# Kernel optimization log

Measured on AMD Instinct MI355X. Metric: run time of the kernel, lower is better.

## Reference

```python
import jax, jax.numpy as jnp
import numpy as np

N, E, D, T = 10000, 320000, 128, 128


def _layer_norm(x, g, b, eps=1e-5):
    mu = jnp.mean(x, axis=-1, keepdims=True)
    var = jnp.mean(jnp.square(x - mu), axis=-1, keepdims=True)
    return (x - mu) * jax.lax.rsqrt(var + eps) * g + b


def setup_inputs() -> dict:
    key = jax.random.key(0)
    ks = jax.random.split(key, 24)
    s = 0.05

    def lin(k, fin, fout):
        k1, k2 = jax.random.split(k)
        return (jax.random.normal(k1, (fin, fout), jnp.float32) * s,
                jax.random.normal(k2, (fout,), jnp.float32) * s)

    W_tp, b_tp = lin(ks[5], T, D)
    W_sg, b_sg = lin(ks[6], D, D)
    W_dg, b_dg = lin(ks[7], D, D)
    W_eg, b_eg = lin(ks[8], D, D)
    W_su, b_su = lin(ks[9], D, D)
    W_du, b_du = lin(ks[10], D, D)
    return {
        'node_feats': jax.random.normal(ks[0], (N, D), jnp.float32),
        'edge_feats': jax.random.normal(ks[1], (E, D), jnp.float32),
        'time_feats': jax.random.normal(ks[2], (N, T), jnp.float32),
        'src': jax.random.randint(ks[3], (E,), 0, N),
        'dst': jax.random.randint(ks[4], (E,), 0, N),
        'W_tp': W_tp, 'b_tp': b_tp,
        'W_sg': W_sg, 'b_sg': b_sg,
        'W_dg': W_dg, 'b_dg': b_dg,
        'W_eg': W_eg, 'b_eg': b_eg,
        'W_su': W_su, 'b_su': b_su,
        'W_du': W_du, 'b_du': b_du,
        'ln_e_g': jnp.ones((D,), jnp.float32), 'ln_e_b': jnp.zeros((D,), jnp.float32),
        'ln_n_g': jnp.ones((D,), jnp.float32), 'ln_n_b': jnp.zeros((D,), jnp.float32),
    }


def reference(node_feats, edge_feats, time_feats, src, dst,
              W_tp, b_tp, W_sg, b_sg, W_dg, b_dg, W_eg, b_eg,
              W_su, b_su, W_du, b_du, ln_e_g, ln_e_b, ln_n_g, ln_n_b):
    n_nodes = node_feats.shape[0]
    # per-node gate projections (time proj folded into source gate)
    e_src = node_feats @ W_sg + b_sg + time_feats @ W_tp + b_tp   # [N, D]
    e_dst = node_feats @ W_dg + b_dg                              # [N, D]
    # edge gating: gather from both endpoints + edge feature projection
    m = e_src[src] + e_dst[dst] + edge_feats @ W_eg + b_eg        # [E, D]
    sigma = jax.nn.sigmoid(m)                                     # [E, D]
    # gated message passing: scatter-add over destination nodes
    Bh = node_feats @ W_du + b_du                                 # [N, D]
    sum_sigma_h = jax.ops.segment_sum(Bh[src] * sigma, dst, num_segments=n_nodes)
    sum_sigma = jax.ops.segment_sum(sigma, dst, num_segments=n_nodes)
    h = sum_sigma_h / (sum_sigma + 1e-6)                          # [N, D]
    x = node_feats @ W_su + b_su + h
    x = jax.nn.silu(_layer_norm(x, ln_n_g, ln_n_b))
    y = jax.nn.silu(_layer_norm(m, ln_e_g, ln_e_b))
    x = node_feats + x  # residual
    y = edge_feats + y
    return (x, y)
```

## Files before the change

### kernel.cpp

```cpp
#include <hip/hip_runtime.h>
#include <hip/hip_bf16.h>

#define N_NODES 10000
#define N_EDGES 320000
#define D 128
#define NBINS 10000

typedef float f32x4 __attribute__((ext_vector_type(4)));
typedef float f32x2 __attribute__((ext_vector_type(2)));
typedef short bf16x8 __attribute__((ext_vector_type(8)));

static __device__ inline short f2bf(float f) {
    union { __hip_bfloat16 h; short s; } u;
    u.h = __float2bfloat16(f);
    return u.s;
}

static __device__ inline float bf2f(short s) {
    union { float f; unsigned u; } x;
    x.u = ((unsigned)(unsigned short)s) << 16;
    return x.f;
}

static __device__ inline float fast_rcp(float x) { return __builtin_amdgcn_rcpf(x); }

__global__ void prepack_kernel(const float* __restrict__ W0, const float* __restrict__ W1,
                               short* __restrict__ out, int K) {
    int idx = blockIdx.x * 256 + threadIdx.x;
    if (idx >= K * 128) return;
    int b  = idx & 7;
    int l  = (idx >> 3) & 63;
    int jt = (idx >> 9) & 7;
    int t  = idx >> 12;
    int k = 32 * t + ((l >> 4) * 8) + b;
    int j = jt * 16 + (l & 15);
    float v = (k < 128) ? W0[k * 128 + j] : W1[(k - 128) * 128 + j];
    out[idx] = f2bf(v);
}

__global__ void hist_kernel(const int* __restrict__ dst, int* __restrict__ cnt) {
    int i = blockIdx.x * 256 + threadIdx.x;
    if (i < N_EDGES) atomicAdd(&cnt[dst[i]], 1);
}

__launch_bounds__(1024)
__global__ void scan_kernel(const int* __restrict__ cnt, int* __restrict__ cursor) {
    __shared__ int s[1024];
    int t = threadIdx.x;
    int b0 = t * 10;
    int loc[10];
    int tot = 0;
#pragma unroll
    for (int i = 0; i < 10; ++i) {
        int v = (b0 + i < NBINS) ? cnt[b0 + i] : 0;
        loc[i] = tot; tot += v;
    }
    s[t] = tot;
    __syncthreads();
    for (int off = 1; off < 1024; off <<= 1) {
        int v = (t >= off) ? s[t - off] : 0;
        __syncthreads();
        s[t] += v;
        __syncthreads();
    }
    int base = (t == 0) ? 0 : s[t - 1];
#pragma unroll
    for (int i = 0; i < 10; ++i)
        if (b0 + i < NBINS) cursor[b0 + i] = base + loc[i];
}

__global__ void scatter_kernel(const int* __restrict__ dst, int* __restrict__ cursor,
                               int* __restrict__ perm) {
    int i = blockIdx.x * 256 + threadIdx.x;
    if (i < N_EDGES) {
        int p = atomicAdd(&cursor[dst[i]], 1);
        perm[p] = i;
    }
}

__launch_bounds__(256)
__global__ void node_proj_kernel(const float* __restrict__ node,
                                 const float* __restrict__ timef,
                                 const short* __restrict__ Wsrc_pk,
                                 const short* __restrict__ Wdg_pk,
                                 const short* __restrict__ Wdu_pk,
                                 const short* __restrict__ Wsu_pk,
                                 const float* __restrict__ b_sg, const float* __restrict__ b_tp,
                                 const float* __restrict__ b_dg, const float* __restrict__ b_du,
                                 const float* __restrict__ b_su, const float* __restrict__ b_eg,
                                 short* __restrict__ spk,
                                 short* __restrict__ dpk,
                                 float* __restrict__ xs) {
    int tid = threadIdx.x;
    int w = tid >> 6;
    int l = tid & 63;
    int g = l >> 4;
    int lr = l & 15;
    int r0 = blockIdx.x * 64 + w * 16;
    int arow = r0 + lr;

    bf16x8 aN[4], aT[4];
    if (arow < N_NODES) {
        const float* np = node + (size_t)arow * D;
        const float* tp = timef + (size_t)arow * D;
#pragma unroll
        for (int t = 0; t < 4; ++t) {
            int k0 = 32 * t + g * 8;
            f32x4 v0 = *(const f32x4*)(np + k0);
            f32x4 v1 = *(const f32x4*)(np + k0 + 4);
            f32x4 u0 = *(const f32x4*)(tp + k0);
            f32x4 u1 = *(const f32x4*)(tp + k0 + 4);
            bf16x8 a, b;
#pragma unroll
            for (int i = 0; i < 4; ++i) {
                a[i] = f2bf(v0[i]); a[4 + i] = f2bf(v1[i]);
                b[i] = f2bf(u0[i]); b[4 + i] = f2bf(u1[i]);
            }
            aN[t] = a; aT[t] = b;
        }
    } else {
        bf16x8 z = {0, 0, 0, 0, 0, 0, 0, 0};
#pragma unroll
        for (int t = 0; t < 4; ++t) { aN[t] = z; aT[t] = z; }
    }

    const bf16x8* Bsrc = (const bf16x8*)Wsrc_pk;
    const bf16x8* Bdg  = (const bf16x8*)Wdg_pk;
    const bf16x8* Bdu  = (const bf16x8*)Wdu_pk;
    const bf16x8* Bsu  = (const bf16x8*)Wsu_pk;

#pragma unroll
    for (int jt = 0; jt < 8; ++jt) {
        int c = jt * 16 + lr;
        f32x4 acc = {0.f, 0.f, 0.f, 0.f};
#pragma unroll
        for (int t = 0; t < 4; ++t)
            acc = __builtin_amdgcn_mfma_f32_16x16x32_bf16(aN[t], Bsrc[(t * 8 + jt) * 64 + l], acc, 0, 0, 0);
#pragma unroll
        for (int t = 0; t < 4; ++t)
            acc = __builtin_amdgcn_mfma_f32_16x16x32_bf16(aT[t], Bsrc[((4 + t) * 8 + jt) * 64 + l], acc, 0, 0, 0);
        float bias = b_sg[c] + b_tp[c];
#pragma unroll
        for (int r = 0; r < 4; ++r) {
            int row = r0 + g * 4 + r;
            if (row < N_NODES) spk[(size_t)row * 256 + c] = f2bf(acc[r] + bias);
        }
    }

#pragma unroll
    for (int jt = 0; jt < 8; ++jt) {
        int c = jt * 16 + lr;
        f32x4 a0 = {0.f, 0.f, 0.f, 0.f}, a1 = a0, a2 = a0;
#pragma unroll
        for (int t = 0; t < 4; ++t) {
            a0 = __builtin_amdgcn_mfma_f32_16x16x32_bf16(aN[t], Bdg[(t * 8 + jt) * 64 + l], a0, 0, 0, 0);
            a1 = __builtin_amdgcn_mfma_f32_16x16x32_bf16(aN[t], Bdu[(t * 8 + jt) * 64 + l], a1, 0, 0, 0);
            a2 = __builtin_amdgcn_mfma_f32_16x16x32_bf16(aN[t], Bsu[(t * 8 + jt) * 64 + l], a2, 0, 0, 0);
        }
        float bdgc = b_dg[c] + b_eg[c];
        float bdu = b_du[c], bsu = b_su[c];
#pragma unroll
        for (int r = 0; r < 4; ++r) {
            int row = r0 + g * 4 + r;
            if (row < N_NODES) {
                dpk[(size_t)row * D + c]       = f2bf(a0[r] + bdgc);
                spk[(size_t)row * 256 + 128 + c] = f2bf(a1[r] + bdu);
                xs[(size_t)row * D + c]        = a2[r] + bsu;
            }
        }
    }
}

__launch_bounds__(256)
__global__ void edge_kernel(const float* __restrict__ edgef,
                            const int* __restrict__ src, const int* __restrict__ dst,
                            const int* __restrict__ perm,
                            const short* __restrict__ Weg_pk,
                            const short* __restrict__ spk,
                            const short* __restrict__ dpk,
                            const float* __restrict__ ln_g, const float* __restrict__ ln_b,
                            float* __restrict__ ss, float* __restrict__ ssh,
                            float* __restrict__ y) {
    __shared__ short Bs[128 * 128];
    {
        const bf16x8* gw = (const bf16x8*)Weg_pk;
        bf16x8* sw = (bf16x8*)Bs;
        for (int i = threadIdx.x; i < 2048; i += 256) sw[i] = gw[i];
    }
    __syncthreads();

    int tid = threadIdx.x;
    int w = tid >> 6;
    int l = tid & 63;
    int g = l >> 4;
    int lr = l & 15;
    int b = blockIdx.x;
    int swz = (b & 7) * 625 + (b >> 3);
    int e0 = swz * 64 + w * 16;

    int eA = perm[e0 + lr];
    int eidx[4], sidx[4], didx[4];
#pragma unroll
    for (int r = 0; r < 4; ++r) {
        eidx[r] = perm[e0 + g * 4 + r];
        sidx[r] = src[eidx[r]];
        didx[r] = dst[eidx[r]];
    }

    bf16x8 aE[4];
    {
        const float* ep = edgef + (size_t)eA * D;
#pragma unroll
        for (int t = 0; t < 4; ++t) {
            int k0 = 32 * t + g * 8;
            f32x4 v0 = *(const f32x4*)(ep + k0);
            f32x4 v1 = *(const f32x4*)(ep + k0 + 4);
            bf16x8 a;
#pragma unroll
            for (int i = 0; i < 4; ++i) { a[i] = f2bf(v0[i]); a[4 + i] = f2bf(v1[i]); }
            aE[t] = a;
        }
    }

    const bf16x8* Bp = (const bf16x8*)Bs;
    f32x4 acc[8];
#pragma unroll
    for (int jt = 0; jt < 8; ++jt) {
        f32x4 c4 = {0.f, 0.f, 0.f, 0.f};
#pragma unroll
        for (int t = 0; t < 4; ++t)
            c4 = __builtin_amdgcn_mfma_f32_16x16x32_bf16(aE[t], Bp[(t * 8 + jt) * 64 + l], c4, 0, 0, 0);
        acc[jt] = c4;
    }

    int dfirst = __shfl(didx[0], 0);
    int dlast  = __shfl(didx[3], 48);
    bool uniform = (dfirst == dlast);

    float gcol[8], bbcol[8];
#pragma unroll
    for (int jt = 0; jt < 8; ++jt) {
        int c = jt * 16 + lr;
        gcol[jt] = ln_g[c]; bbcol[jt] = ln_b[c];
    }

    float sum[4] = {0.f, 0.f, 0.f, 0.f}, sq[4] = {0.f, 0.f, 0.f, 0.f};
#pragma unroll
    for (int jt = 0; jt < 8; ++jt) {
        int c = jt * 16 + lr;
        float sg[4], bsg[4];
#pragma unroll
        for (int r = 0; r < 4; ++r) {
            float es = bf2f(spk[(size_t)sidx[r] * 256 + c]);
            float bh = bf2f(spk[(size_t)sidx[r] * 256 + 128 + c]);
            float ed = bf2f(dpk[(size_t)didx[r] * D + c]);
            float m = acc[jt][r] + es + ed;
            acc[jt][r] = m;
            float s = fast_rcp(1.f + __expf(-m));
            sg[r] = s;
            bsg[r] = bh * s;
            sum[r] += m; sq[r] += m * m;
        }
        if (uniform) {
            float aS = (sg[0] + sg[1]) + (sg[2] + sg[3]);
            float aH = (bsg[0] + bsg[1]) + (bsg[2] + bsg[3]);
            aS += __shfl_xor(aS, 16); aH += __shfl_xor(aH, 16);
            aS += __shfl_xor(aS, 32); aH += __shfl_xor(aH, 32);
            if (g == 0) {
                atomicAdd(&ss [(size_t)dfirst * D + c], aS);
                atomicAdd(&ssh[(size_t)dfirst * D + c], aH);
            }
        } else {
            float aS = sg[0], aH = bsg[0];
#pragma unroll
            for (int r = 1; r < 4; ++r) {
                if (didx[r] == didx[r - 1]) { aS += sg[r]; aH += bsg[r]; }
                else {
                    atomicAdd(&ss [(size_t)didx[r - 1] * D + c], aS);
                    atomicAdd(&ssh[(size_t)didx[r - 1] * D + c], aH);
                    aS = sg[r]; aH = bsg[r];
                }
            }
            atomicAdd(&ss [(size_t)didx[3] * D + c], aS);
            atomicAdd(&ssh[(size_t)didx[3] * D + c], aH);
        }
    }

#pragma unroll
    for (int r = 0; r < 4; ++r) {
        float s = sum[r], q = sq[r];
#pragma unroll
        for (int mk = 1; mk < 16; mk <<= 1) { s += __shfl_xor(s, mk); q += __shfl_xor(q, mk); }
        float mean = s * (1.f / D);
        float var = q * (1.f / D) - mean * mean;
        sum[r] = mean;
        sq[r] = rsqrtf(var + 1e-5f);
    }

#pragma unroll
    for (int jt = 0; jt < 8; ++jt) {
        int c = jt * 16 + lr;
#pragma unroll
        for (int r = 0; r < 4; ++r) {
            float v = (acc[jt][r] - sum[r]) * sq[r] * gcol[jt] + bbcol[jt];
            float sl = v * fast_rcp(1.f + __expf(-v));
            size_t off = (size_t)eidx[r] * D + c;
            y[off] = edgef[off] + sl;
        }
    }
}

__launch_bounds__(256)
__global__ void node_out_kernel(const float* __restrict__ node,
                                const float* __restrict__ xs,
                                const float* __restrict__ ssh, const float* __restrict__ ss,
                                const float* __restrict__ ln_g, const float* __restrict__ ln_b,
                                float* __restrict__ x) {
    int w = threadIdx.x >> 6;
    int l = threadIdx.x & 63;
    int row = blockIdx.x * 4 + w;
    if (row >= N_NODES) return;
    size_t base = (size_t)row * D + 2 * l;
    f32x2 xv = *(const f32x2*)(xs + base);
    f32x2 hs = *(const f32x2*)(ssh + base);
    f32x2 sv = *(const f32x2*)(ss + base);
    float v0 = xv[0] + hs[0] / (sv[0] + 1e-6f);
    float v1 = xv[1] + hs[1] / (sv[1] + 1e-6f);
    float s = v0 + v1, q = v0 * v0 + v1 * v1;
#pragma unroll
    for (int mk = 1; mk < 64; mk <<= 1) { s += __shfl_xor(s, mk); q += __shfl_xor(q, mk); }
    float mean = s * (1.f / D);
    float var = q * (1.f / D) - mean * mean;
    float rstd = rsqrtf(var + 1e-5f);
    float t0 = (v0 - mean) * rstd * ln_g[2 * l] + ln_b[2 * l];
    float t1 = (v1 - mean) * rstd * ln_g[2 * l + 1] + ln_b[2 * l + 1];
    t0 = t0 * fast_rcp(1.f + __expf(-t0));
    t1 = t1 * fast_rcp(1.f + __expf(-t1));
    f32x2 nv = *(const f32x2*)(node + base);
    f32x2 outv;
    outv[0] = nv[0] + t0;
    outv[1] = nv[1] + t1;
    *(f32x2*)(x + base) = outv;
}

extern "C" void kernel_launch(void* const* d_in, const int* in_sizes, int n_in,
                              void* d_out, int out_size, void* d_ws, size_t ws_size,
                              hipStream_t stream) {
    const float* node  = (const float*)d_in[0];
    const float* edgef = (const float*)d_in[1];
    const float* timef = (const float*)d_in[2];
    const int*   src   = (const int*)d_in[3];
    const int*   dst   = (const int*)d_in[4];
    const float* W_tp = (const float*)d_in[5];  const float* b_tp = (const float*)d_in[6];
    const float* W_sg = (const float*)d_in[7];  const float* b_sg = (const float*)d_in[8];
    const float* W_dg = (const float*)d_in[9];  const float* b_dg = (const float*)d_in[10];
    const float* W_eg = (const float*)d_in[11]; const float* b_eg = (const float*)d_in[12];
    const float* W_su = (const float*)d_in[13]; const float* b_su = (const float*)d_in[14];
    const float* W_du = (const float*)d_in[15]; const float* b_du = (const float*)d_in[16];
    const float* ln_e_g = (const float*)d_in[17]; const float* ln_e_b = (const float*)d_in[18];
    const float* ln_n_g = (const float*)d_in[19]; const float* ln_n_b = (const float*)d_in[20];

    char* ws = (char*)d_ws;
    size_t nd = (size_t)N_NODES * D;
    float* ss    = (float*)ws; ws += nd * 4;
    float* ssh   = (float*)ws; ws += nd * 4;
    float* xs    = (float*)ws; ws += nd * 4;
    short* spk   = (short*)ws; ws += (size_t)N_NODES * 256 * 2;
    short* dpk   = (short*)ws; ws += nd * 2;
    short* Wsrc_pk = (short*)ws; ws += 256 * 128 * 2;
    short* Wdg_pk  = (short*)ws; ws += 128 * 128 * 2;
    short* Wdu_pk  = (short*)ws; ws += 128 * 128 * 2;
    short* Wsu_pk  = (short*)ws; ws += 128 * 128 * 2;
    short* Weg_pk  = (short*)ws; ws += 128 * 128 * 2;
    int* cnt       = (int*)ws; ws += 10240 * 4;
    int* cursor    = (int*)ws; ws += 10240 * 4;
    int* perm      = (int*)ws; ws += (size_t)N_EDGES * 4;

    hipMemsetAsync(ss, 0, 2 * nd * 4, stream);
    hipMemsetAsync(cnt, 0, 10240 * 4, stream);

    hist_kernel<<<(N_EDGES + 255) / 256, 256, 0, stream>>>(dst, cnt);
    scan_kernel<<<1, 1024, 0, stream>>>(cnt, cursor);
    scatter_kernel<<<(N_EDGES + 255) / 256, 256, 0, stream>>>(dst, cursor, perm);

    prepack_kernel<<<128, 256, 0, stream>>>(W_sg, W_tp, Wsrc_pk, 256);
    prepack_kernel<<<64, 256, 0, stream>>>(W_dg, W_dg, Wdg_pk, 128);
    prepack_kernel<<<64, 256, 0, stream>>>(W_du, W_du, Wdu_pk, 128);
    prepack_kernel<<<64, 256, 0, stream>>>(W_su, W_su, Wsu_pk, 128);
    prepack_kernel<<<64, 256, 0, stream>>>(W_eg, W_eg, Weg_pk, 128);

    node_proj_kernel<<<(N_NODES + 63) / 64, 256, 0, stream>>>(
        node, timef, Wsrc_pk, Wdg_pk, Wdu_pk, Wsu_pk,
        b_sg, b_tp, b_dg, b_du, b_su, b_eg, spk, dpk, xs);

    edge_kernel<<<N_EDGES / 64, 256, 0, stream>>>(
        edgef, src, dst, perm, Weg_pk, spk, dpk,
        ln_e_g, ln_e_b, ss, ssh, (float*)d_out + nd);

    node_out_kernel<<<N_NODES / 4, 256, 0, stream>>>(
        node, xs, ssh, ss, ln_n_g, ln_n_b, (float*)d_out);
}
```

Measured before the change: 291.0 us.

## Permute node projection layout for vectorized edge gathers and presort src/dst indices

Node projections are now stored in a column-interleaved bf16 layout. Each edge lane can then fetch its eight columns for the source, update and destination vectors with one 16-byte load instead of many scalar 2-byte gathers. The scatter pass also writes src and dst in dst-sorted order, so the edge kernel reads them contiguously rather than through perm. The five weight-prepack launches are merged into one, and edge outputs use nontemporal stores. The cost is extra workspace and writes for the sorted index arrays, plus more live registers in the edge kernel.

```diff
diff --git a/kernel.cpp b/kernel.cpp
--- a/kernel.cpp
+++ b/kernel.cpp
@@ -24,18 +24,27 @@
 
 static __device__ inline float fast_rcp(float x) { return __builtin_amdgcn_rcpf(x); }
 
-__global__ void prepack_kernel(const float* __restrict__ W0, const float* __restrict__ W1,
-                               short* __restrict__ out, int K) {
+__global__ void prepack_all(const float* __restrict__ W_sg, const float* __restrict__ W_tp,
+                            const float* __restrict__ W_dg, const float* __restrict__ W_du,
+                            const float* __restrict__ W_su, const float* __restrict__ W_eg,
+                            short* __restrict__ Wsrc, short* __restrict__ Wdg,
+                            short* __restrict__ Wdu, short* __restrict__ Wsu,
+                            short* __restrict__ Weg) {
     int idx = blockIdx.x * 256 + threadIdx.x;
-    if (idx >= K * 128) return;
-    int b  = idx & 7;
-    int l  = (idx >> 3) & 63;
-    int jt = (idx >> 9) & 7;
-    int t  = idx >> 12;
+    const float* W0; const float* W1; short* out; int i2;
+    if (idx < 32768)      { W0 = W_sg; W1 = W_tp; out = Wsrc; i2 = idx; }
+    else if (idx < 49152) { W0 = W_dg; W1 = W_dg; out = Wdg;  i2 = idx - 32768; }
+    else if (idx < 65536) { W0 = W_du; W1 = W_du; out = Wdu;  i2 = idx - 49152; }
+    else if (idx < 81920) { W0 = W_su; W1 = W_su; out = Wsu;  i2 = idx - 65536; }
+    else                  { W0 = W_eg; W1 = W_eg; out = Weg;  i2 = idx - 81920; }
+    int b  = i2 & 7;
+    int l  = (i2 >> 3) & 63;
+    int jt = (i2 >> 9) & 7;
+    int t  = i2 >> 12;
     int k = 32 * t + ((l >> 4) * 8) + b;
     int j = jt * 16 + (l & 15);
     float v = (k < 128) ? W0[k * 128 + j] : W1[(k - 128) * 128 + j];
-    out[idx] = f2bf(v);
+    out[i2] = f2bf(v);
 }
 
 __global__ void hist_kernel(const int* __restrict__ dst, int* __restrict__ cnt) {
@@ -69,12 +78,17 @@
         if (b0 + i < NBINS) cursor[b0 + i] = base + loc[i];
 }
 
-__global__ void scatter_kernel(const int* __restrict__ dst, int* __restrict__ cursor,
-                               int* __restrict__ perm) {
+__global__ void scatter_kernel(const int* __restrict__ src, const int* __restrict__ dst,
+                               int* __restrict__ cursor,
+                               int* __restrict__ perm,
+                               int* __restrict__ src_s, int* __restrict__ dst_s) {
     int i = blockIdx.x * 256 + threadIdx.x;
     if (i < N_EDGES) {
-        int p = atomicAdd(&cursor[dst[i]], 1);
+        int d = dst[i];
+        int p = atomicAdd(&cursor[d], 1);
         perm[p] = i;
+        src_s[p] = src[i];
+        dst_s[p] = d;
     }
 }
 
@@ -129,43 +143,60 @@
     const bf16x8* Bdu  = (const bf16x8*)Wdu_pk;
     const bf16x8* Bsu  = (const bf16x8*)Wsu_pk;
 
-#pragma unroll
-    for (int jt = 0; jt < 8; ++jt) {
-        int c = jt * 16 + lr;
-        f32x4 acc = {0.f, 0.f, 0.f, 0.f};
-#pragma unroll
-        for (int t = 0; t < 4; ++t)
-            acc = __builtin_amdgcn_mfma_f32_16x16x32_bf16(aN[t], Bsrc[(t * 8 + jt) * 64 + l], acc, 0, 0, 0);
-#pragma unroll
-        for (int t = 0; t < 4; ++t)
-            acc = __builtin_amdgcn_mfma_f32_16x16x32_bf16(aT[t], Bsrc[((4 + t) * 8 + jt) * 64 + l], acc, 0, 0, 0);
-        float bias = b_sg[c] + b_tp[c];
+    {
+        bf16x8 chunk[4];
+#pragma unroll
+        for (int jt = 0; jt < 8; ++jt) {
+            int c = jt * 16 + lr;
+            f32x4 acc = {0.f, 0.f, 0.f, 0.f};
+#pragma unroll
+            for (int t = 0; t < 4; ++t)
+                acc = __builtin_amdgcn_mfma_f32_16x16x32_bf16(aN[t], Bsrc[(t * 8 + jt) * 64 + l], acc, 0, 0, 0);
+#pragma unroll
+            for (int t = 0; t < 4; ++t)
+                acc = __builtin_amdgcn_mfma_f32_16x16x32_bf16(aT[t], Bsrc[((4 + t) * 8 + jt) * 64 + l], acc, 0, 0, 0);
+            float bias = b_sg[c] + b_tp[c];
+#pragma unroll
+            for (int r = 0; r < 4; ++r) chunk[r][jt] = f2bf(acc[r] + bias);
+        }
 #pragma unroll
         for (int r = 0; r < 4; ++r) {
             int row = r0 + g * 4 + r;
-            if (row < N_NODES) spk[(size_t)row * 256 + c] = f2bf(acc[r] + bias);
-        }
-    }
-
-#pragma unroll
-    for (int jt = 0; jt < 8; ++jt) {
-        int c = jt * 16 + lr;
-        f32x4 a0 = {0.f, 0.f, 0.f, 0.f}, a1 = a0, a2 = a0;
-#pragma unroll
-        for (int t = 0; t < 4; ++t) {
-            a0 = __builtin_amdgcn_mfma_f32_16x16x32_bf16(aN[t], Bdg[(t * 8 + jt) * 64 + l], a0, 0, 0, 0);
-            a1 = __builtin_amdgcn_mfma_f32_16x16x32_bf16(aN[t], Bdu[(t * 8 + jt) * 64 + l], a1, 0, 0, 0);
-            a2 = __builtin_amdgcn_mfma_f32_16x16x32_bf16(aN[t], Bsu[(t * 8 + jt) * 64 + l], a2, 0, 0, 0);
-        }
-        float bdgc = b_dg[c] + b_eg[c];
-        float bdu = b_du[c], bsu = b_su[c];
+            if (row < N_NODES) *(bf16x8*)(spk + (size_t)row * 256 + lr * 8) = chunk[r];
+        }
+    }
+
+    {
+        bf16x8 chD[4], chH[4];
+        float xsv[4][8];
+#pragma unroll
+        for (int jt = 0; jt < 8; ++jt) {
+            int c = jt * 16 + lr;
+            f32x4 a0 = {0.f, 0.f, 0.f, 0.f}, a1 = a0, a2 = a0;
+#pragma unroll
+            for (int t = 0; t < 4; ++t) {
+                a0 = __builtin_amdgcn_mfma_f32_16x16x32_bf16(aN[t], Bdg[(t * 8 + jt) * 64 + l], a0, 0, 0, 0);
+                a1 = __builtin_amdgcn_mfma_f32_16x16x32_bf16(aN[t], Bdu[(t * 8 + jt) * 64 + l], a1, 0, 0, 0);
+                a2 = __builtin_amdgcn_mfma_f32_16x16x32_bf16(aN[t], Bsu[(t * 8 + jt) * 64 + l], a2, 0, 0, 0);
+            }
+            float bdgc = b_dg[c] + b_eg[c];
+            float bdu = b_du[c], bsu = b_su[c];
+#pragma unroll
+            for (int r = 0; r < 4; ++r) {
+                chD[r][jt] = f2bf(a0[r] + bdgc);
+                chH[r][jt] = f2bf(a1[r] + bdu);
+                xsv[r][jt] = a2[r] + bsu;
+            }
+        }
 #pragma unroll
         for (int r = 0; r < 4; ++r) {
             int row = r0 + g * 4 + r;
             if (row < N_NODES) {
-                dpk[(size_t)row * D + c]       = f2bf(a0[r] + bdgc);
-                spk[(size_t)row * 256 + 128 + c] = f2bf(a1[r] + bdu);
-                xs[(size_t)row * D + c]        = a2[r] + bsu;
+                *(bf16x8*)(dpk + (size_t)row * D + lr * 8) = chD[r];
+                *(bf16x8*)(spk + (size_t)row * 256 + 128 + lr * 8) = chH[r];
+#pragma unroll
+                for (int jt = 0; jt < 8; ++jt)
+                    xs[(size_t)row * D + jt * 16 + lr] = xsv[r][jt];
             }
         }
     }
@@ -173,8 +204,8 @@
 
 __launch_bounds__(256)
 __global__ void edge_kernel(const float* __restrict__ edgef,
-                            const int* __restrict__ src, const int* __restrict__ dst,
                             const int* __restrict__ perm,
+                            const int* __restrict__ src_s, const int* __restrict__ dst_s,
                             const short* __restrict__ Weg_pk,
                             const short* __restrict__ spk,
                             const short* __restrict__ dpk,
@@ -203,8 +234,16 @@
 #pragma unroll
     for (int r = 0; r < 4; ++r) {
         eidx[r] = perm[e0 + g * 4 + r];
-        sidx[r] = src[eidx[r]];
-        didx[r] = dst[eidx[r]];
+        sidx[r] = src_s[e0 + g * 4 + r];
+        didx[r] = dst_s[e0 + g * 4 + r];
+    }
+
+    bf16x8 esv[4], bhv[4], edv[4];
+#pragma unroll
+    for (int r = 0; r < 4; ++r) {
+        esv[r] = *(const bf16x8*)(spk + (size_t)sidx[r] * 256 + lr * 8);
+        bhv[r] = *(const bf16x8*)(spk + (size_t)sidx[r] * 256 + 128 + lr * 8);
+        edv[r] = *(const bf16x8*)(dpk + (size_t)didx[r] * D + lr * 8);
     }
 
     bf16x8 aE[4];
@@ -237,13 +276,6 @@
     int dlast  = __shfl(didx[3], 48);
     bool uniform = (dfirst == dlast);
 
-    float gcol[8], bbcol[8];
-#pragma unroll
-    for (int jt = 0; jt < 8; ++jt) {
-        int c = jt * 16 + lr;
-        gcol[jt] = ln_g[c]; bbcol[jt] = ln_b[c];
-    }
-
     float sum[4] = {0.f, 0.f, 0.f, 0.f}, sq[4] = {0.f, 0.f, 0.f, 0.f};
 #pragma unroll
     for (int jt = 0; jt < 8; ++jt) {
@@ -251,14 +283,11 @@
         float sg[4], bsg[4];
 #pragma unroll
         for (int r = 0; r < 4; ++r) {
-            float es = bf2f(spk[(size_t)sidx[r] * 256 + c]);
-            float bh = bf2f(spk[(size_t)sidx[r] * 256 + 128 + c]);
-            float ed = bf2f(dpk[(size_t)didx[r] * D + c]);
-            float m = acc[jt][r] + es + ed;
+            float m = acc[jt][r] + bf2f(esv[r][jt]) + bf2f(edv[r][jt]);
             acc[jt][r] = m;
             float s = fast_rcp(1.f + __expf(-m));
             sg[r] = s;
-            bsg[r] = bh * s;
+            bsg[r] = bf2f(bhv[r][jt]) * s;
             sum[r] += m; sq[r] += m * m;
         }
         if (uniform) {
@@ -300,12 +329,13 @@
 #pragma unroll
     for (int jt = 0; jt < 8; ++jt) {
         int c = jt * 16 + lr;
+        float gc = ln_g[c], bc = ln_b[c];
 #pragma unroll
         for (int r = 0; r < 4; ++r) {
-            float v = (acc[jt][r] - sum[r]) * sq[r] * gcol[jt] + bbcol[jt];
+            float v = (acc[jt][r] - sum[r]) * sq[r] * gc + bc;
             float sl = v * fast_rcp(1.f + __expf(-v));
             size_t off = (size_t)eidx[r] * D + c;
-            y[off] = edgef[off] + sl;
+            __builtin_nontemporal_store(edgef[off] + sl, &y[off]);
         }
     }
 }
@@ -375,26 +405,25 @@
     int* cnt       = (int*)ws; ws += 10240 * 4;
     int* cursor    = (int*)ws; ws += 10240 * 4;
     int* perm      = (int*)ws; ws += (size_t)N_EDGES * 4;
+    int* src_s     = (int*)ws; ws += (size_t)N_EDGES * 4;
+    int* dst_s     = (int*)ws; ws += (size_t)N_EDGES * 4;
 
     hipMemsetAsync(ss, 0, 2 * nd * 4, stream);
     hipMemsetAsync(cnt, 0, 10240 * 4, stream);
 
     hist_kernel<<<(N_EDGES + 255) / 256, 256, 0, stream>>>(dst, cnt);
     scan_kernel<<<1, 1024, 0, stream>>>(cnt, cursor);
-    scatter_kernel<<<(N_EDGES + 255) / 256, 256, 0, stream>>>(dst, cursor, perm);
-
-    prepack_kernel<<<128, 256, 0, stream>>>(W_sg, W_tp, Wsrc_pk, 256);
-    prepack_kernel<<<64, 256, 0, stream>>>(W_dg, W_dg, Wdg_pk, 128);
-    prepack_kernel<<<64, 256, 0, stream>>>(W_du, W_du, Wdu_pk, 128);
-    prepack_kernel<<<64, 256, 0, stream>>>(W_su, W_su, Wsu_pk, 128);
-    prepack_kernel<<<64, 256, 0, stream>>>(W_eg, W_eg, Weg_pk, 128);
+    scatter_kernel<<<(N_EDGES + 255) / 256, 256, 0, stream>>>(src, dst, cursor, perm, src_s, dst_s);
+
+    prepack_all<<<384, 256, 0, stream>>>(W_sg, W_tp, W_dg, W_du, W_su, W_eg,
+                                         Wsrc_pk, Wdg_pk, Wdu_pk, Wsu_pk, Weg_pk);
 
     node_proj_kernel<<<(N_NODES + 63) / 64, 256, 0, stream>>>(
         node, timef, Wsrc_pk, Wdg_pk, Wdu_pk, Wsu_pk,
         b_sg, b_tp, b_dg, b_du, b_su, b_eg, spk, dpk, xs);
 
     edge_kernel<<<N_EDGES / 64, 256, 0, stream>>>(
-        edgef, src, dst, perm, Weg_pk, spk, dpk,
+        edgef, perm, src_s, dst_s, Weg_pk, spk, dpk,
         ln_e_g, ln_e_b, ss, ssh, (float*)d_out + nd);
 
     node_out_kernel<<<N_NODES / 4, 256, 0, stream>>>(
```

After: 245.2 us. 1.19x faster.
